# Kernel optimization log

Hardware: AMD Instinct MI355X
Metric: run time of the kernel (lower is better)

## Reference

```python
import jax, jax.numpy as jnp
import numpy as np

N = 1000000
E = 16000000


def gcn_conv(x, W, b, src, dst, dinv_sqrt):
    # x: [N, Cin]; W: [Cin, Cout]; src/dst: [E'] (self-loops included)
    xw = x @ W                                   # [N, Cout]
    norm = dinv_sqrt[src] * dinv_sqrt[dst]       # [E']
    msg = xw[src] * norm[:, None]                # [E', Cout]
    out = jax.ops.segment_sum(msg, dst, num_segments=x.shape[0])
    return out + b


def setup_inputs() -> dict:
    key = jax.random.key(0)
    ks = jax.random.split(key, 8)
    x = jax.random.normal(ks[0], (N, 1), dtype=jnp.float32)
    edge_index = jax.random.randint(ks[1], (2, E), 0, N, dtype=jnp.int64)
    W1 = jax.random.normal(ks[2], (1, 3), dtype=jnp.float32)
    b1 = jax.random.normal(ks[3], (3,), dtype=jnp.float32) * 0.1
    W2 = jax.random.normal(ks[4], (3, 3), dtype=jnp.float32) * 0.5
    b2 = jax.random.normal(ks[5], (3,), dtype=jnp.float32) * 0.1
    W3 = jax.random.normal(ks[6], (3, 3), dtype=jnp.float32) * 0.5
    b3 = jax.random.normal(ks[7], (3,), dtype=jnp.float32) * 0.1
    return {"x": x, "edge_index": edge_index, "W1": W1, "b1": b1,
            "W2": W2, "b2": b2, "W3": W3, "b3": b3}


def reference(x, edge_index, W1, b1, W2, b2, W3, b3):
    n = x.shape[0]
    # add self-loops (PyG GCNConv default)
    loop = jnp.arange(n, dtype=edge_index.dtype)
    src = jnp.concatenate([edge_index[0], loop])
    dst = jnp.concatenate([edge_index[1], loop])
    # symmetric normalization: deg over targets of A + I
    deg = jax.ops.segment_sum(jnp.ones_like(dst, dtype=x.dtype), dst, num_segments=n)
    dinv_sqrt = jnp.where(deg > 0, jax.lax.rsqrt(deg), 0.0)
    h = jax.nn.relu(gcn_conv(x, W1, b1, src, dst, dinv_sqrt))
    h = jax.nn.relu(gcn_conv(h, W2, b2, src, dst, dinv_sqrt))
    h = jax.nn.relu(gcn_conv(h, W3, b3, src, dst, dinv_sqrt))
    return h
```

## Files before the change

kernel.cpp:

```cpp
#include <hip/hip_runtime.h>

#define THREADS 256
#define TILE 8192
#define TPB_S 512
#define EPT 16
#define BUCKET_BITS 10
#define BUCKET_SIZE 1024
#define NT_MAX 2048
#define STAGE_CAP 16512
#define NSLICE 8
#define SLICE_SHIFT 17

__device__ __forceinline__ long long llmin(long long a, long long b) { return a < b ? a : b; }


__global__ void detect_i64_kernel(const int* __restrict__ e, int* __restrict__ flag) {
    if (blockIdx.x == 0 && threadIdx.x == 0) {
        bool all_odd_zero = true, any_even = false;
#pragma unroll
        for (int k = 0; k < 16; ++k) {
            if (e[2 * k + 1] != 0) all_odd_zero = false;
            if (e[2 * k] != 0) any_even = true;
        }
        *flag = (all_odd_zero && any_even) ? 1 : 0;
    }
}


__global__ __launch_bounds__(TPB_S) void binsort_kernel(
        const int* __restrict__ e, long long E, const int* __restrict__ flag,
        int nbuck, int* __restrict__ packed, int* __restrict__ ofs) {
    __shared__ int hist[1024];
    __shared__ int sarr[TPB_S];
    __shared__ int srec[TILE];
    const int tid = threadIdx.x;
    hist[tid] = 0;
    hist[tid + TPB_S] = 0;
    __syncthreads();

    const bool i64 = (*flag != 0);
    const long long beg = (long long)blockIdx.x * TILE;
    const int tile_len = (int)llmin((long long)TILE, E - beg);

    int rec[EPT];
    int bkt[EPT];
#pragma unroll
    for (int k = 0; k < EPT; ++k) {
        int j = tid + k * TPB_S;
        bkt[k] = -1;
        if (j < tile_len) {
            long long idx = beg + j;
            int s, d;
            if (i64) { s = ((const int2*)e)[idx].x; d = ((const int2*)e)[E + idx].x; }
            else     { s = e[idx];                  d = e[E + idx]; }
            bkt[k] = d >> BUCKET_BITS;
            rec[k] = ((d & (BUCKET_SIZE - 1)) << 20) | s;
            atomicAdd(&hist[bkt[k]], 1);
        }
    }
    __syncthreads();

    int v0 = hist[2 * tid], v1 = hist[2 * tid + 1];
    sarr[tid] = v0 + v1;
    __syncthreads();
    for (int off = 1; off < TPB_S; off <<= 1) {
        int t = (tid >= off) ? sarr[tid - off] : 0;
        __syncthreads();
        sarr[tid] += t;
        __syncthreads();
    }
    int excl = (tid == 0) ? 0 : sarr[tid - 1];
    hist[2 * tid] = excl;
    hist[2 * tid + 1] = excl + v0;
    __syncthreads();

    int* orow = ofs + (size_t)blockIdx.x * nbuck;
    if (tid < nbuck) orow[tid] = hist[tid];
    if (tid + TPB_S < nbuck) orow[tid + TPB_S] = hist[tid + TPB_S];
    __syncthreads();

#pragma unroll
    for (int k = 0; k < EPT; ++k) {
        if (bkt[k] >= 0) {
            int pos = atomicAdd(&hist[bkt[k]], 1);
            srec[pos] = rec[k];
        }
    }
    __syncthreads();

    int* prow = packed + (size_t)blockIdx.x * TILE;
    for (int j = tid; j < tile_len; j += TPB_S) prow[j] = srec[j];
}

#define TRT 32
__global__ void transpose_kernel(const int* __restrict__ in, int rows, int cols,
                                 int* __restrict__ outT) {
    __shared__ int tb[TRT][TRT + 1];
    int c0 = blockIdx.x * TRT, r0 = blockIdx.y * TRT;
    int lx = threadIdx.x, ly = threadIdx.y;
    for (int dy = ly; dy < TRT; dy += 8) {
        int r = r0 + dy, c = c0 + lx;
        if (r < rows && c < cols) tb[dy][lx] = in[(size_t)r * cols + c];
    }
    __syncthreads();
    for (int dy = ly; dy < TRT; dy += 8) {
        int r = c0 + dy, c = r0 + lx;
        if (r < cols && c < rows) outT[(size_t)r * rows + c] = tb[lx][dy];
    }
}


__global__ __launch_bounds__(THREADS) void bcnt_kernel(
        const int* __restrict__ ofsT, long long E, int ntiles, int nbuck,
        int* __restrict__ bcnt) {
    __shared__ int sh[THREADS];
    const int b = blockIdx.x, tid = threadIdx.x;
    const int* row0 = ofsT + (size_t)b * ntiles;
    const int* row1 = row0 + ntiles;
    const bool last_b = (b == nbuck - 1);
    int s = 0;
    for (int t = tid; t < ntiles; t += THREADS) {
        int o = row0[t];
        int tl = (t == ntiles - 1) ? (int)(E - (long long)t * TILE) : TILE;
        int o2 = last_b ? tl : row1[t];
        s += o2 - o;
    }
    sh[tid] = s;
    __syncthreads();
    for (int off = THREADS >> 1; off > 0; off >>= 1) {
        if (tid < off) sh[tid] += sh[tid + off];
        __syncthreads();
    }
    if (tid == 0) bcnt[b] = sh[0];
}

__global__ __launch_bounds__(1024) void bscan_kernel(
        const int* __restrict__ bcnt, int nbuck, int* __restrict__ bs) {
    __shared__ int sh[1024];
    int tid = threadIdx.x;
    int v = (tid < nbuck) ? bcnt[tid] : 0;
    sh[tid] = v;
    __syncthreads();
    for (int off = 1; off < 1024; off <<= 1) {
        int t = (tid >= off) ? sh[tid - off] : 0;
        __syncthreads();
        sh[tid] += t;
        __syncthreads();
    }
    if (tid < nbuck) bs[tid] = sh[tid] - v;
    if (tid == nbuck - 1) bs[nbuck] = sh[tid];
}


__global__ __launch_bounds__(TPB_S) void merge_kernel(
        const int* __restrict__ ofsT, const int* __restrict__ packed,
        const int* __restrict__ bs, long long E, int ntiles, int nbuck,
        int* __restrict__ merged) {
    __shared__ int lofs[NT_MAX];
    __shared__ int tsum[TPB_S];
    __shared__ int stage[STAGE_CAP];
    __shared__ int stage2[STAGE_CAP];
    __shared__ int scnt[NSLICE];
    __shared__ int scur[NSLICE];
    const int tid = threadIdx.x, b = blockIdx.x;
    const int* row0 = ofsT + (size_t)b * ntiles;
    const int* row1 = row0 + ntiles;
    const bool last_b = (b == nbuck - 1);
    const int per = (ntiles + TPB_S - 1) / TPB_S;
    const int t0 = tid * per;
    if (tid < NSLICE) scnt[tid] = 0;

    int s = 0;
    for (int k = 0; k < per; ++k) {
        int t = t0 + k;
        if (t < ntiles) {
            int o = row0[t];
            int tl = (t == ntiles - 1) ? (int)(E - (long long)t * TILE) : TILE;
            int o2 = last_b ? tl : row1[t];
            lofs[t] = s;
            s += o2 - o;
        }
    }
    tsum[tid] = s;
    __syncthreads();
    for (int off = 1; off < TPB_S; off <<= 1) {
        int t = (tid >= off) ? tsum[tid - off] : 0;
        __syncthreads();
        tsum[tid] += t;
        __syncthreads();
    }
    const int excl = tsum[tid] - s;
    const int total = tsum[TPB_S - 1];
    for (int k = 0; k < per; ++k) {
        int t = t0 + k;
        if (t < ntiles) lofs[t] += excl;
    }
    __syncthreads();

    const int bsb = bs[b];
    int myslc[NSLICE];
#pragma unroll
    for (int i = 0; i < NSLICE; ++i) myslc[i] = 0;

    for (int k = 0; k < per; ++k) {
        int t = t0 + k;
        if (t >= ntiles) break;
        int o = row0[t];
        int tl = (t == ntiles - 1) ? (int)(E - (long long)t * TILE) : TILE;
        int o2 = last_b ? tl : row1[t];
        const int* pr = packed + (size_t)t * TILE;
        int q = lofs[t];
        for (int j = o; j < o2; ++j, ++q) {
            int a0 = pr[j];
            if (q < STAGE_CAP) {
                stage[q] = a0;
                myslc[((unsigned)a0 & 0xFFFFFu) >> SLICE_SHIFT]++;
            } else {
                merged[bsb + q] = a0;
            }
        }
    }
#pragma unroll
    for (int i = 0; i < NSLICE; ++i)
        if (myslc[i]) atomicAdd(&scnt[i], myslc[i]);
    __syncthreads();
    if (tid == 0) {
        int run = 0;
#pragma unroll
        for (int i = 0; i < NSLICE; ++i) { scur[i] = run; run += scnt[i]; }
    }
    __syncthreads();

    const int wlen = total < STAGE_CAP ? total : STAGE_CAP;
    for (int j = tid; j < wlen; j += TPB_S) {
        int rec = stage[j];
        int sl = ((unsigned)rec & 0xFFFFFu) >> SLICE_SHIFT;
        int pos = atomicAdd(&scur[sl], 1);
        stage2[pos] = rec;
    }
    __syncthreads();
    for (int j = tid; j < wlen; j += TPB_S) merged[bsb + j] = stage2[j];
}


__global__ __launch_bounds__(TPB_S) void deg_init_kernel(
        const int* __restrict__ bs, const int* __restrict__ packed,
        const float* __restrict__ x,
        float* __restrict__ dinv, float* __restrict__ p, int N) {
    __shared__ int cnt[BUCKET_SIZE];
    for (int k = threadIdx.x; k < BUCKET_SIZE; k += blockDim.x) cnt[k] = 0;
    __syncthreads();
    int beg = bs[blockIdx.x], end = bs[blockIdx.x + 1];
    int stride = blockDim.x;
    int k = beg + threadIdx.x;
    for (; k + 3 * stride < end; k += 4 * stride) {
        unsigned r0 = packed[k], r1 = packed[k + stride];
        unsigned r2 = packed[k + 2 * stride], r3 = packed[k + 3 * stride];
        atomicAdd(&cnt[r0 >> 20], 1);
        atomicAdd(&cnt[r1 >> 20], 1);
        atomicAdd(&cnt[r2 >> 20], 1);
        atomicAdd(&cnt[r3 >> 20], 1);
    }
    for (; k < end; k += stride) atomicAdd(&cnt[((unsigned)packed[k]) >> 20], 1);
    __syncthreads();
    int base = blockIdx.x << BUCKET_BITS;
    for (int j = threadIdx.x; j < BUCKET_SIZE; j += blockDim.x) {
        int i = base + j;
        if (i < N) {
            float di = rsqrtf((float)cnt[j] + 1.0f);
            dinv[i] = di;
            p[i] = x[i] * di;
        }
    }
}

__global__ __launch_bounds__(TPB_S) void layer1_bucket_kernel(
        const int* __restrict__ bs, const int* __restrict__ packed,
        const float* __restrict__ p, const float* __restrict__ dinv,
        const float* __restrict__ W1, const float* __restrict__ b1,
        const float* __restrict__ W2,
        float4* __restrict__ y2, int N) {
    __shared__ float acc[BUCKET_SIZE];
    for (int k = threadIdx.x; k < BUCKET_SIZE; k += blockDim.x) acc[k] = 0.0f;
    __syncthreads();
    int beg = bs[blockIdx.x], end = bs[blockIdx.x + 1];
    int stride = blockDim.x;
    int k = beg + threadIdx.x;
    for (; k + 3 * stride < end; k += 4 * stride) {
        unsigned r0 = packed[k], r1 = packed[k + stride];
        unsigned r2 = packed[k + 2 * stride], r3 = packed[k + 3 * stride];
        float v0 = p[r0 & 0xFFFFFu], v1 = p[r1 & 0xFFFFFu];
        float v2 = p[r2 & 0xFFFFFu], v3 = p[r3 & 0xFFFFFu];
        atomicAdd(&acc[r0 >> 20], v0);
        atomicAdd(&acc[r1 >> 20], v1);
        atomicAdd(&acc[r2 >> 20], v2);
        atomicAdd(&acc[r3 >> 20], v3);
    }
    for (; k < end; k += stride) {
        unsigned rec = (unsigned)packed[k];
        atomicAdd(&acc[rec >> 20], p[rec & 0xFFFFFu]);
    }
    __syncthreads();
    int base = blockIdx.x << BUCKET_BITS;
    for (int j = threadIdx.x; j < BUCKET_SIZE; j += blockDim.x) {
        int i = base + j;
        if (i >= N) continue;
        float di = dinv[i];
        float t = di * (acc[j] + p[i]);
        float h0 = fmaxf(t * W1[0] + b1[0], 0.0f);
        float h1 = fmaxf(t * W1[1] + b1[1], 0.0f);
        float h2 = fmaxf(t * W1[2] + b1[2], 0.0f);
        float4 o;
        o.x = di * (h0 * W2[0] + h1 * W2[3] + h2 * W2[6]);
        o.y = di * (h0 * W2[1] + h1 * W2[4] + h2 * W2[7]);
        o.z = di * (h0 * W2[2] + h1 * W2[5] + h2 * W2[8]);
        o.w = 0.0f;
        y2[i] = o;
    }
}

__global__ __launch_bounds__(TPB_S) void layer_mid_bucket_kernel(
        const int* __restrict__ bs, const int* __restrict__ packed,
        const float4* __restrict__ y, const float* __restrict__ dinv,
        const float* __restrict__ b, const float* __restrict__ Wn,
        float4* __restrict__ ynext, int N) {
    __shared__ float acc[BUCKET_SIZE * 3];
    for (int k = threadIdx.x; k < BUCKET_SIZE * 3; k += blockDim.x) acc[k] = 0.0f;
    __syncthreads();
    int beg = bs[blockIdx.x], end = bs[blockIdx.x + 1];
    int stride = blockDim.x;
    int k = beg + threadIdx.x;
    for (; k + 3 * stride < end; k += 4 * stride) {
        unsigned r0 = packed[k], r1 = packed[k + stride];
        unsigned r2 = packed[k + 2 * stride], r3 = packed[k + 3 * stride];
        float4 v0 = y[r0 & 0xFFFFFu], v1 = y[r1 & 0xFFFFFu];
        float4 v2 = y[r2 & 0xFFFFFu], v3 = y[r3 & 0xFFFFFu];
        int d0 = (r0 >> 20) * 3, d1 = (r1 >> 20) * 3, d2 = (r2 >> 20) * 3, d3 = (r3 >> 20) * 3;
        atomicAdd(&acc[d0 + 0], v0.x); atomicAdd(&acc[d0 + 1], v0.y); atomicAdd(&acc[d0 + 2], v0.z);
        atomicAdd(&acc[d1 + 0], v1.x); atomicAdd(&acc[d1 + 1], v1.y); atomicAdd(&acc[d1 + 2], v1.z);
        atomicAdd(&acc[d2 + 0], v2.x); atomicAdd(&acc[d2 + 1], v2.y); atomicAdd(&acc[d2 + 2], v2.z);
        atomicAdd(&acc[d3 + 0], v3.x); atomicAdd(&acc[d3 + 1], v3.y); atomicAdd(&acc[d3 + 2], v3.z);
    }
    for (; k < end; k += stride) {
        unsigned rec = (unsigned)packed[k];
        float4 v = y[rec & 0xFFFFFu];
        int dl = (rec >> 20) * 3;
        atomicAdd(&acc[dl + 0], v.x);
        atomicAdd(&acc[dl + 1], v.y);
        atomicAdd(&acc[dl + 2], v.z);
    }
    __syncthreads();
    int base = blockIdx.x << BUCKET_BITS;
    for (int j = threadIdx.x; j < BUCKET_SIZE; j += blockDim.x) {
        int i = base + j;
        if (i >= N) continue;
        float di = dinv[i];
        float4 yi = y[i];
        float h0 = fmaxf(di * (acc[j * 3 + 0] + yi.x) + b[0], 0.0f);
        float h1 = fmaxf(di * (acc[j * 3 + 1] + yi.y) + b[1], 0.0f);
        float h2 = fmaxf(di * (acc[j * 3 + 2] + yi.z) + b[2], 0.0f);
        float4 o;
        o.x = di * (h0 * Wn[0] + h1 * Wn[3] + h2 * Wn[6]);
        o.y = di * (h0 * Wn[1] + h1 * Wn[4] + h2 * Wn[7]);
        o.z = di * (h0 * Wn[2] + h1 * Wn[5] + h2 * Wn[8]);
        o.w = 0.0f;
        ynext[i] = o;
    }
}

__global__ __launch_bounds__(TPB_S) void layer_last_bucket_kernel(
        const int* __restrict__ bs, const int* __restrict__ packed,
        const float4* __restrict__ y, const float* __restrict__ dinv,
        const float* __restrict__ b,
        float* __restrict__ out, int N) {
    __shared__ float acc[BUCKET_SIZE * 3];
    for (int k = threadIdx.x; k < BUCKET_SIZE * 3; k += blockDim.x) acc[k] = 0.0f;
    __syncthreads();
    int beg = bs[blockIdx.x], end = bs[blockIdx.x + 1];
    int stride = blockDim.x;
    int k = beg + threadIdx.x;
    for (; k + 3 * stride < end; k += 4 * stride) {
        unsigned r0 = packed[k], r1 = packed[k + stride];
        unsigned r2 = packed[k + 2 * stride], r3 = packed[k + 3 * stride];
        float4 v0 = y[r0 & 0xFFFFFu], v1 = y[r1 & 0xFFFFFu];
        float4 v2 = y[r2 & 0xFFFFFu], v3 = y[r3 & 0xFFFFFu];
        int d0 = (r0 >> 20) * 3, d1 = (r1 >> 20) * 3, d2 = (r2 >> 20) * 3, d3 = (r3 >> 20) * 3;
        atomicAdd(&acc[d0 + 0], v0.x); atomicAdd(&acc[d0 + 1], v0.y); atomicAdd(&acc[d0 + 2], v0.z);
        atomicAdd(&acc[d1 + 0], v1.x); atomicAdd(&acc[d1 + 1], v1.y); atomicAdd(&acc[d1 + 2], v1.z);
        atomicAdd(&acc[d2 + 0], v2.x); atomicAdd(&acc[d2 + 1], v2.y); atomicAdd(&acc[d2 + 2], v2.z);
        atomicAdd(&acc[d3 + 0], v3.x); atomicAdd(&acc[d3 + 1], v3.y); atomicAdd(&acc[d3 + 2], v3.z);
    }
    for (; k < end; k += stride) {
        unsigned rec = (unsigned)packed[k];
        float4 v = y[rec & 0xFFFFFu];
        int dl = (rec >> 20) * 3;
        atomicAdd(&acc[dl + 0], v.x);
        atomicAdd(&acc[dl + 1], v.y);
        atomicAdd(&acc[dl + 2], v.z);
    }
    __syncthreads();
    int base = blockIdx.x << BUCKET_BITS;
    for (int j = threadIdx.x; j < BUCKET_SIZE; j += blockDim.x) {
        int i = base + j;
        if (i >= N) continue;
        float di = dinv[i];
        float4 yi = y[i];
        out[i * 3 + 0] = fmaxf(di * (acc[j * 3 + 0] + yi.x) + b[0], 0.0f);
        out[i * 3 + 1] = fmaxf(di * (acc[j * 3 + 1] + yi.y) + b[1], 0.0f);
        out[i * 3 + 2] = fmaxf(di * (acc[j * 3 + 2] + yi.z) + b[2], 0.0f);
    }
}


__global__ void deg_kernel(const int* __restrict__ e, long long E,
                           const int* __restrict__ flag, float* __restrict__ deg) {
    const bool i64 = (*flag != 0);
    long long i = (long long)blockIdx.x * blockDim.x + threadIdx.x;
    const long long stride = (long long)gridDim.x * blockDim.x;
    for (; i < E; i += stride) {
        long long t = i64 ? (long long)e[2 * E + 2 * i] : (long long)e[E + i];
        atomicAdd(deg + t, 1.0f);
    }
}

__global__ void node_init_kernel(const float* __restrict__ x, const float* __restrict__ W1,
                                 float* __restrict__ deg_dinv, float* __restrict__ A, int N) {
    int i = blockIdx.x * blockDim.x + threadIdx.x;
    if (i >= N) return;
    float di = rsqrtf(deg_dinv[i] + 1.0f);
    deg_dinv[i] = di;
    float v = x[i] * di;
    A[i * 3 + 0] = v * W1[0];
    A[i * 3 + 1] = v * W1[1];
    A[i * 3 + 2] = v * W1[2];
}

__global__ void scatter_kernel(const int* __restrict__ e, long long E,
                               const int* __restrict__ flag,
                               const float* __restrict__ y, float* __restrict__ acc) {
    const bool i64 = (*flag != 0);
    long long i = (long long)blockIdx.x * blockDim.x + threadIdx.x;
    const long long stride = (long long)gridDim.x * blockDim.x;
    for (; i < E; i += stride) {
        int s, t;
        if (i64) { s = e[2 * i]; t = e[2 * E + 2 * i]; }
        else     { s = e[i];     t = e[E + i]; }
        atomicAdd(acc + (long long)t * 3 + 0, y[(long long)s * 3 + 0]);
        atomicAdd(acc + (long long)t * 3 + 1, y[(long long)s * 3 + 1]);
        atomicAdd(acc + (long long)t * 3 + 2, y[(long long)s * 3 + 2]);
    }
}

__global__ void finalize_mid_kernel(const float* __restrict__ dinv, const float* __restrict__ y,
                                    float* __restrict__ acc, const float* __restrict__ b,
                                    const float* __restrict__ Wn, int N) {
    int i = blockIdx.x * blockDim.x + threadIdx.x;
    if (i >= N) return;
    float di = dinv[i];
    float h0 = fmaxf(di * (acc[i * 3 + 0] + y[i * 3 + 0]) + b[0], 0.0f);
    float h1 = fmaxf(di * (acc[i * 3 + 1] + y[i * 3 + 1]) + b[1], 0.0f);
    float h2 = fmaxf(di * (acc[i * 3 + 2] + y[i * 3 + 2]) + b[2], 0.0f);
    float z0 = di * (h0 * Wn[0] + h1 * Wn[3] + h2 * Wn[6]);
    float z1 = di * (h0 * Wn[1] + h1 * Wn[4] + h2 * Wn[7]);
    float z2 = di * (h0 * Wn[2] + h1 * Wn[5] + h2 * Wn[8]);
    acc[i * 3 + 0] = z0;
    acc[i * 3 + 1] = z1;
    acc[i * 3 + 2] = z2;
}

__global__ void finalize_last_kernel(const float* __restrict__ dinv, const float* __restrict__ y,
                                     const float* __restrict__ acc, const float* __restrict__ b,
                                     float* __restrict__ out, int N) {
    int i = blockIdx.x * blockDim.x + threadIdx.x;
    if (i >= N) return;
    float di = dinv[i];
    out[i * 3 + 0] = fmaxf(di * (acc[i * 3 + 0] + y[i * 3 + 0]) + b[0], 0.0f);
    out[i * 3 + 1] = fmaxf(di * (acc[i * 3 + 1] + y[i * 3 + 1]) + b[1], 0.0f);
    out[i * 3 + 2] = fmaxf(di * (acc[i * 3 + 2] + y[i * 3 + 2]) + b[2], 0.0f);
}


extern "C" void kernel_launch(void* const* d_in, const int* in_sizes, int n_in,
                              void* d_out, int out_size, void* d_ws, size_t ws_size,
                              hipStream_t stream) {
    const float* x  = (const float*)d_in[0];
    const int*   ei = (const int*)d_in[1];
    const float* W1 = (const float*)d_in[2];
    const float* b1 = (const float*)d_in[3];
    const float* W2 = (const float*)d_in[4];
    const float* b2 = (const float*)d_in[5];
    const float* W3 = (const float*)d_in[6];
    const float* b3 = (const float*)d_in[7];
    float* out = (float*)d_out;

    const long long N = in_sizes[0];
    const long long E = (long long)in_sizes[1] / 2;

    const int nbuck  = (int)((N + BUCKET_SIZE - 1) >> BUCKET_BITS);
    const int ntiles = (int)((E + TILE - 1) / TILE);

    char* w = (char*)d_ws;
    size_t off = 0;
    auto alloc = [&](size_t bytes) -> char* {
        char* pp = w + off;
        off = (off + bytes + 255) & ~(size_t)255;
        return pp;
    };

    int*    flag   = (int*)alloc(4);
    int*    ofs    = (int*)alloc((size_t)ntiles * nbuck * 4);
    int*    ofsT   = (int*)alloc((size_t)nbuck * ntiles * 4);
    int*    bcnt   = (int*)alloc((size_t)nbuck * 4);
    int*    bs     = (int*)alloc(((size_t)nbuck + 1) * 4);
    int*    packed = (int*)alloc((size_t)ntiles * TILE * 4);
    int*    merged = (int*)alloc((size_t)E * 4);
    float*  dinv   = (float*)alloc((size_t)N * 4);
    float*  p      = (float*)alloc((size_t)N * 4);
    float4* y2     = (float4*)packed;
    float4* y3     = (float4*)((char*)packed + (size_t)N * 16);

    const int nblk = (int)((N + THREADS - 1) / THREADS);

    if (off <= ws_size && N <= (1 << 20) && nbuck <= 1024 && ntiles <= NT_MAX &&
        (size_t)ntiles * TILE * 4 >= (size_t)N * 32) {
        detect_i64_kernel<<<1, 64, 0, stream>>>(ei, flag);
        binsort_kernel<<<ntiles, TPB_S, 0, stream>>>(ei, E, flag, nbuck, packed, ofs);
        dim3 tb(32, 8);
        dim3 tg((nbuck + TRT - 1) / TRT, (ntiles + TRT - 1) / TRT);
        transpose_kernel<<<tg, tb, 0, stream>>>(ofs, ntiles, nbuck, ofsT);
        bcnt_kernel<<<nbuck, THREADS, 0, stream>>>(ofsT, E, ntiles, nbuck, bcnt);
        bscan_kernel<<<1, 1024, 0, stream>>>(bcnt, nbuck, bs);
        merge_kernel<<<nbuck, TPB_S, 0, stream>>>(ofsT, packed, bs, E, ntiles, nbuck, merged);

        deg_init_kernel<<<nbuck, TPB_S, 0, stream>>>(bs, merged, x, dinv, p, (int)N);
        layer1_bucket_kernel<<<nbuck, TPB_S, 0, stream>>>(bs, merged, p, dinv, W1, b1, W2, y2, (int)N);
        layer_mid_bucket_kernel<<<nbuck, TPB_S, 0, stream>>>(bs, merged, y2, dinv, b2, W3, y3, (int)N);
        layer_last_bucket_kernel<<<nbuck, TPB_S, 0, stream>>>(bs, merged, y3, dinv, b3, out, (int)N);
    } else {
        int*   fflag = (int*)w;
        float* fdinv = (float*)(w + 256);
        float* A     = fdinv + N;
        size_t need_full = 256 + (size_t)N * 4 + (size_t)N * 12 * 2;
        float* B = (ws_size >= need_full) ? (A + 3 * N) : out;
        const int eblk = 2048;

        detect_i64_kernel<<<1, 64, 0, stream>>>(ei, fflag);
        hipMemsetAsync(fdinv, 0, (size_t)N * 4, stream);
        deg_kernel<<<eblk, THREADS, 0, stream>>>(ei, E, fflag, fdinv);
        node_init_kernel<<<nblk, THREADS, 0, stream>>>(x, W1, fdinv, A, (int)N);

        hipMemsetAsync(B, 0, (size_t)N * 12, stream);
        scatter_kernel<<<eblk, THREADS, 0, stream>>>(ei, E, fflag, A, B);
        finalize_mid_kernel<<<nblk, THREADS, 0, stream>>>(fdinv, A, B, b1, W2, (int)N);

        hipMemsetAsync(A, 0, (size_t)N * 12, stream);
        scatter_kernel<<<eblk, THREADS, 0, stream>>>(ei, E, fflag, B, A);
        finalize_mid_kernel<<<nblk, THREADS, 0, stream>>>(fdinv, B, A, b2, W3, (int)N);

        hipMemsetAsync(B, 0, (size_t)N * 12, stream);
        scatter_kernel<<<eblk, THREADS, 0, stream>>>(ei, E, fflag, A, B);
        finalize_last_kernel<<<nblk, THREADS, 0, stream>>>(fdinv, A, B, b3, out, (int)N);
    }
}
```

Baseline: 904.9 us.

## Rewrite merge as count-then-scatter and vectorize edge loads in bucket kernels

The merge kernel no longer copies records into a staging buffer and then reorders them with shared atomics. It first counts records per source slice for each thread, runs a block prefix scan to get each thread's private write cursors, then scatters directly into one staging array. This drops one shared buffer and the atomic reordering pass, at the cost of reading the packed tiles twice. The degree and layer kernels now read edge records as aligned int4 pairs with eight gathers in flight per thread, which adds alignment prologue and epilogue loops and changes the per-thread access pattern from strided to contiguous chunks.

```diff
diff --git a/kernel.cpp b/kernel.cpp
--- a/kernel.cpp
+++ b/kernel.cpp
@@ -7,9 +7,10 @@
 #define BUCKET_BITS 10
 #define BUCKET_SIZE 1024
 #define NT_MAX 2048
-#define STAGE_CAP 16512
 #define NSLICE 8
 #define SLICE_SHIFT 17
+#define CAP2 17408
+#define MSK 0xFFFFFu
 
 __device__ __forceinline__ long long llmin(long long a, long long b) { return a < b ? a : b; }
 
@@ -156,51 +157,19 @@
         const int* __restrict__ ofsT, const int* __restrict__ packed,
         const int* __restrict__ bs, long long E, int ntiles, int nbuck,
         int* __restrict__ merged) {
-    __shared__ int lofs[NT_MAX];
-    __shared__ int tsum[TPB_S];
-    __shared__ int stage[STAGE_CAP];
-    __shared__ int stage2[STAGE_CAP];
-    __shared__ int scnt[NSLICE];
-    __shared__ int scur[NSLICE];
+    __shared__ int stage2[CAP2];
+    __shared__ int f[NSLICE * TPB_S];
+    __shared__ int sarr[TPB_S];
     const int tid = threadIdx.x, b = blockIdx.x;
     const int* row0 = ofsT + (size_t)b * ntiles;
     const int* row1 = row0 + ntiles;
     const bool last_b = (b == nbuck - 1);
     const int per = (ntiles + TPB_S - 1) / TPB_S;
     const int t0 = tid * per;
-    if (tid < NSLICE) scnt[tid] = 0;
-
-    int s = 0;
-    for (int k = 0; k < per; ++k) {
-        int t = t0 + k;
-        if (t < ntiles) {
-            int o = row0[t];
-            int tl = (t == ntiles - 1) ? (int)(E - (long long)t * TILE) : TILE;
-            int o2 = last_b ? tl : row1[t];
-            lofs[t] = s;
-            s += o2 - o;
-        }
-    }
-    tsum[tid] = s;
-    __syncthreads();
-    for (int off = 1; off < TPB_S; off <<= 1) {
-        int t = (tid >= off) ? tsum[tid - off] : 0;
-        __syncthreads();
-        tsum[tid] += t;
-        __syncthreads();
-    }
-    const int excl = tsum[tid] - s;
-    const int total = tsum[TPB_S - 1];
-    for (int k = 0; k < per; ++k) {
-        int t = t0 + k;
-        if (t < ntiles) lofs[t] += excl;
-    }
-    __syncthreads();
-
-    const int bsb = bs[b];
-    int myslc[NSLICE];
-#pragma unroll
-    for (int i = 0; i < NSLICE; ++i) myslc[i] = 0;
+
+    int cnt[NSLICE];
+#pragma unroll
+    for (int i = 0; i < NSLICE; ++i) cnt[i] = 0;
 
     for (int k = 0; k < per; ++k) {
         int t = t0 + k;
@@ -209,63 +178,89 @@
         int tl = (t == ntiles - 1) ? (int)(E - (long long)t * TILE) : TILE;
         int o2 = last_b ? tl : row1[t];
         const int* pr = packed + (size_t)t * TILE;
-        int q = lofs[t];
-        for (int j = o; j < o2; ++j, ++q) {
-            int a0 = pr[j];
-            if (q < STAGE_CAP) {
-                stage[q] = a0;
-                myslc[((unsigned)a0 & 0xFFFFFu) >> SLICE_SHIFT]++;
-            } else {
-                merged[bsb + q] = a0;
-            }
+        for (int j = o; j < o2; ++j)
+            cnt[(((unsigned)pr[j]) & MSK) >> SLICE_SHIFT]++;
+    }
+#pragma unroll
+    for (int sl = 0; sl < NSLICE; ++sl) f[sl * TPB_S + tid] = cnt[sl];
+    __syncthreads();
+
+    int loc[NSLICE];
+    int s = 0;
+#pragma unroll
+    for (int j = 0; j < NSLICE; ++j) { loc[j] = f[tid * NSLICE + j]; s += loc[j]; }
+    sarr[tid] = s;
+    __syncthreads();
+    for (int off = 1; off < TPB_S; off <<= 1) {
+        int t = (tid >= off) ? sarr[tid - off] : 0;
+        __syncthreads();
+        sarr[tid] += t;
+        __syncthreads();
+    }
+    int ex = sarr[tid] - s;
+    const int total = sarr[TPB_S - 1];
+#pragma unroll
+    for (int j = 0; j < NSLICE; ++j) { f[tid * NSLICE + j] = ex; ex += loc[j]; }
+    __syncthreads();
+
+    int cur[NSLICE];
+#pragma unroll
+    for (int sl = 0; sl < NSLICE; ++sl) cur[sl] = f[sl * TPB_S + tid];
+
+    const int bsb = bs[b];
+    for (int k = 0; k < per; ++k) {
+        int t = t0 + k;
+        if (t >= ntiles) break;
+        int o = row0[t];
+        int tl = (t == ntiles - 1) ? (int)(E - (long long)t * TILE) : TILE;
+        int o2 = last_b ? tl : row1[t];
+        const int* pr = packed + (size_t)t * TILE;
+        for (int j = o; j < o2; ++j) {
+            int r = pr[j];
+            int sl = (((unsigned)r) & MSK) >> SLICE_SHIFT;
+            int pos = cur[sl]++;
+            if (pos < CAP2) stage2[pos] = r;
+            else merged[bsb + pos] = r;
         }
     }
-#pragma unroll
-    for (int i = 0; i < NSLICE; ++i)
-        if (myslc[i]) atomicAdd(&scnt[i], myslc[i]);
-    __syncthreads();
-    if (tid == 0) {
-        int run = 0;
-#pragma unroll
-        for (int i = 0; i < NSLICE; ++i) { scur[i] = run; run += scnt[i]; }
-    }
-    __syncthreads();
-
-    const int wlen = total < STAGE_CAP ? total : STAGE_CAP;
-    for (int j = tid; j < wlen; j += TPB_S) {
-        int rec = stage[j];
-        int sl = ((unsigned)rec & 0xFFFFFu) >> SLICE_SHIFT;
-        int pos = atomicAdd(&scur[sl], 1);
-        stage2[pos] = rec;
-    }
-    __syncthreads();
+    __syncthreads();
+    const int wlen = total < CAP2 ? total : CAP2;
     for (int j = tid; j < wlen; j += TPB_S) merged[bsb + j] = stage2[j];
 }
 
 
 __global__ __launch_bounds__(TPB_S) void deg_init_kernel(
-        const int* __restrict__ bs, const int* __restrict__ packed,
+        const int* __restrict__ bs, const int* __restrict__ merged,
         const float* __restrict__ x,
         float* __restrict__ dinv, float* __restrict__ p, int N) {
     __shared__ int cnt[BUCKET_SIZE];
-    for (int k = threadIdx.x; k < BUCKET_SIZE; k += blockDim.x) cnt[k] = 0;
+    const int tid = threadIdx.x;
+    for (int k = tid; k < BUCKET_SIZE; k += TPB_S) cnt[k] = 0;
     __syncthreads();
     int beg = bs[blockIdx.x], end = bs[blockIdx.x + 1];
-    int stride = blockDim.x;
-    int k = beg + threadIdx.x;
-    for (; k + 3 * stride < end; k += 4 * stride) {
-        unsigned r0 = packed[k], r1 = packed[k + stride];
-        unsigned r2 = packed[k + 2 * stride], r3 = packed[k + 3 * stride];
-        atomicAdd(&cnt[r0 >> 20], 1);
-        atomicAdd(&cnt[r1 >> 20], 1);
-        atomicAdd(&cnt[r2 >> 20], 1);
-        atomicAdd(&cnt[r3 >> 20], 1);
-    }
-    for (; k < end; k += stride) atomicAdd(&cnt[((unsigned)packed[k]) >> 20], 1);
-    __syncthreads();
-    int base = blockIdx.x << BUCKET_BITS;
-    for (int j = threadIdx.x; j < BUCKET_SIZE; j += blockDim.x) {
-        int i = base + j;
+    int a0 = (beg + 3) & ~3; if (a0 > end) a0 = end;
+    for (int k = beg + tid; k < a0; k += TPB_S)
+        atomicAdd(&cnt[((unsigned)merged[k]) >> 20], 1);
+    int base = a0;
+    for (; base + 8 * TPB_S <= end; base += 8 * TPB_S) {
+        int q = base + tid * 8;
+        int4 ra = *(const int4*)(merged + q);
+        int4 rb = *(const int4*)(merged + q + 4);
+        atomicAdd(&cnt[((unsigned)ra.x) >> 20], 1);
+        atomicAdd(&cnt[((unsigned)ra.y) >> 20], 1);
+        atomicAdd(&cnt[((unsigned)ra.z) >> 20], 1);
+        atomicAdd(&cnt[((unsigned)ra.w) >> 20], 1);
+        atomicAdd(&cnt[((unsigned)rb.x) >> 20], 1);
+        atomicAdd(&cnt[((unsigned)rb.y) >> 20], 1);
+        atomicAdd(&cnt[((unsigned)rb.z) >> 20], 1);
+        atomicAdd(&cnt[((unsigned)rb.w) >> 20], 1);
+    }
+    for (int k = base + tid; k < end; k += TPB_S)
+        atomicAdd(&cnt[((unsigned)merged[k]) >> 20], 1);
+    __syncthreads();
+    int nbase = blockIdx.x << BUCKET_BITS;
+    for (int j = tid; j < BUCKET_SIZE; j += TPB_S) {
+        int i = nbase + j;
         if (i < N) {
             float di = rsqrtf((float)cnt[j] + 1.0f);
             dinv[i] = di;
@@ -275,35 +270,51 @@
 }
 
 __global__ __launch_bounds__(TPB_S) void layer1_bucket_kernel(
-        const int* __restrict__ bs, const int* __restrict__ packed,
+        const int* __restrict__ bs, const int* __restrict__ merged,
         const float* __restrict__ p, const float* __restrict__ dinv,
         const float* __restrict__ W1, const float* __restrict__ b1,
         const float* __restrict__ W2,
         float4* __restrict__ y2, int N) {
     __shared__ float acc[BUCKET_SIZE];
-    for (int k = threadIdx.x; k < BUCKET_SIZE; k += blockDim.x) acc[k] = 0.0f;
+    const int tid = threadIdx.x;
+    for (int k = tid; k < BUCKET_SIZE; k += TPB_S) acc[k] = 0.0f;
     __syncthreads();
     int beg = bs[blockIdx.x], end = bs[blockIdx.x + 1];
-    int stride = blockDim.x;
-    int k = beg + threadIdx.x;
-    for (; k + 3 * stride < end; k += 4 * stride) {
-        unsigned r0 = packed[k], r1 = packed[k + stride];
-        unsigned r2 = packed[k + 2 * stride], r3 = packed[k + 3 * stride];
-        float v0 = p[r0 & 0xFFFFFu], v1 = p[r1 & 0xFFFFFu];
-        float v2 = p[r2 & 0xFFFFFu], v3 = p[r3 & 0xFFFFFu];
-        atomicAdd(&acc[r0 >> 20], v0);
-        atomicAdd(&acc[r1 >> 20], v1);
-        atomicAdd(&acc[r2 >> 20], v2);
-        atomicAdd(&acc[r3 >> 20], v3);
-    }
-    for (; k < end; k += stride) {
-        unsigned rec = (unsigned)packed[k];
-        atomicAdd(&acc[rec >> 20], p[rec & 0xFFFFFu]);
-    }
-    __syncthreads();
-    int base = blockIdx.x << BUCKET_BITS;
-    for (int j = threadIdx.x; j < BUCKET_SIZE; j += blockDim.x) {
-        int i = base + j;
+    int a0 = (beg + 3) & ~3; if (a0 > end) a0 = end;
+    for (int k = beg + tid; k < a0; k += TPB_S) {
+        unsigned r = (unsigned)merged[k];
+        atomicAdd(&acc[r >> 20], p[r & MSK]);
+    }
+    int base = a0;
+    for (; base + 8 * TPB_S <= end; base += 8 * TPB_S) {
+        int q = base + tid * 8;
+        int4 ra = *(const int4*)(merged + q);
+        int4 rb = *(const int4*)(merged + q + 4);
+        float v0 = p[((unsigned)ra.x) & MSK];
+        float v1 = p[((unsigned)ra.y) & MSK];
+        float v2 = p[((unsigned)ra.z) & MSK];
+        float v3 = p[((unsigned)ra.w) & MSK];
+        float v4 = p[((unsigned)rb.x) & MSK];
+        float v5 = p[((unsigned)rb.y) & MSK];
+        float v6 = p[((unsigned)rb.z) & MSK];
+        float v7 = p[((unsigned)rb.w) & MSK];
+        atomicAdd(&acc[((unsigned)ra.x) >> 20], v0);
+        atomicAdd(&acc[((unsigned)ra.y) >> 20], v1);
+        atomicAdd(&acc[((unsigned)ra.z) >> 20], v2);
+        atomicAdd(&acc[((unsigned)ra.w) >> 20], v3);
+        atomicAdd(&acc[((unsigned)rb.x) >> 20], v4);
+        atomicAdd(&acc[((unsigned)rb.y) >> 20], v5);
+        atomicAdd(&acc[((unsigned)rb.z) >> 20], v6);
+        atomicAdd(&acc[((unsigned)rb.w) >> 20], v7);
+    }
+    for (int k = base + tid; k < end; k += TPB_S) {
+        unsigned r = (unsigned)merged[k];
+        atomicAdd(&acc[r >> 20], p[r & MSK]);
+    }
+    __syncthreads();
+    int nbase = blockIdx.x << BUCKET_BITS;
+    for (int j = tid; j < BUCKET_SIZE; j += TPB_S) {
+        int i = nbase + j;
         if (i >= N) continue;
         float di = dinv[i];
         float t = di * (acc[j] + p[i]);
@@ -319,40 +330,58 @@
     }
 }
 
+__device__ __forceinline__ void acc3_atomic(float* acc, unsigned r, float4 v) {
+    int dl = (r >> 20) * 3;
+    atomicAdd(&acc[dl + 0], v.x);
+    atomicAdd(&acc[dl + 1], v.y);
+    atomicAdd(&acc[dl + 2], v.z);
+}
+
 __global__ __launch_bounds__(TPB_S) void layer_mid_bucket_kernel(
-        const int* __restrict__ bs, const int* __restrict__ packed,
+        const int* __restrict__ bs, const int* __restrict__ merged,
         const float4* __restrict__ y, const float* __restrict__ dinv,
         const float* __restrict__ b, const float* __restrict__ Wn,
         float4* __restrict__ ynext, int N) {
     __shared__ float acc[BUCKET_SIZE * 3];
-    for (int k = threadIdx.x; k < BUCKET_SIZE * 3; k += blockDim.x) acc[k] = 0.0f;
+    const int tid = threadIdx.x;
+    for (int k = tid; k < BUCKET_SIZE * 3; k += TPB_S) acc[k] = 0.0f;
     __syncthreads();
     int beg = bs[blockIdx.x], end = bs[blockIdx.x + 1];
-    int stride = blockDim.x;
-    int k = beg + threadIdx.x;
-    for (; k + 3 * stride < end; k += 4 * stride) {
-        unsigned r0 = packed[k], r1 = packed[k + stride];
-        unsigned r2 = packed[k + 2 * stride], r3 = packed[k + 3 * stride];
-        float4 v0 = y[r0 & 0xFFFFFu], v1 = y[r1 & 0xFFFFFu];
-        float4 v2 = y[r2 & 0xFFFFFu], v3 = y[r3 & 0xFFFFFu];
-        int d0 = (r0 >> 20) * 3, d1 = (r1 >> 20) * 3, d2 = (r2 >> 20) * 3, d3 = (r3 >> 20) * 3;
-        atomicAdd(&acc[d0 + 0], v0.x); atomicAdd(&acc[d0 + 1], v0.y); atomicAdd(&acc[d0 + 2], v0.z);
-        atomicAdd(&acc[d1 + 0], v1.x); atomicAdd(&acc[d1 + 1], v1.y); atomicAdd(&acc[d1 + 2], v1.z);
-        atomicAdd(&acc[d2 + 0], v2.x); atomicAdd(&acc[d2 + 1], v2.y); atomicAdd(&acc[d2 + 2], v2.z);
-        atomicAdd(&acc[d3 + 0], v3.x); atomicAdd(&acc[d3 + 1], v3.y); atomicAdd(&acc[d3 + 2], v3.z);
-    }
-    for (; k < end; k += stride) {
-        unsigned rec = (unsigned)packed[k];
-        float4 v = y[rec & 0xFFFFFu];
-        int dl = (rec >> 20) * 3;
-        atomicAdd(&acc[dl + 0], v.x);
-        atomicAdd(&acc[dl + 1], v.y);
-        atomicAdd(&acc[dl + 2], v.z);
-    }
-    __syncthreads();
-    int base = blockIdx.x << BUCKET_BITS;
-    for (int j = threadIdx.x; j < BUCKET_SIZE; j += blockDim.x) {
-        int i = base + j;
+    int a0 = (beg + 3) & ~3; if (a0 > end) a0 = end;
+    for (int k = beg + tid; k < a0; k += TPB_S) {
+        unsigned r = (unsigned)merged[k];
+        acc3_atomic(acc, r, y[r & MSK]);
+    }
+    int base = a0;
+    for (; base + 8 * TPB_S <= end; base += 8 * TPB_S) {
+        int q = base + tid * 8;
+        int4 ra = *(const int4*)(merged + q);
+        int4 rb = *(const int4*)(merged + q + 4);
+        float4 v0 = y[((unsigned)ra.x) & MSK];
+        float4 v1 = y[((unsigned)ra.y) & MSK];
+        float4 v2 = y[((unsigned)ra.z) & MSK];
+        float4 v3 = y[((unsigned)ra.w) & MSK];
+        float4 v4 = y[((unsigned)rb.x) & MSK];
+        float4 v5 = y[((unsigned)rb.y) & MSK];
+        float4 v6 = y[((unsigned)rb.z) & MSK];
+        float4 v7 = y[((unsigned)rb.w) & MSK];
+        acc3_atomic(acc, (unsigned)ra.x, v0);
+        acc3_atomic(acc, (unsigned)ra.y, v1);
+        acc3_atomic(acc, (unsigned)ra.z, v2);
+        acc3_atomic(acc, (unsigned)ra.w, v3);
+        acc3_atomic(acc, (unsigned)rb.x, v4);
+        acc3_atomic(acc, (unsigned)rb.y, v5);
+        acc3_atomic(acc, (unsigned)rb.z, v6);
+        acc3_atomic(acc, (unsigned)rb.w, v7);
+    }
+    for (int k = base + tid; k < end; k += TPB_S) {
+        unsigned r = (unsigned)merged[k];
+        acc3_atomic(acc, r, y[r & MSK]);
+    }
+    __syncthreads();
+    int nbase = blockIdx.x << BUCKET_BITS;
+    for (int j = tid; j < BUCKET_SIZE; j += TPB_S) {
+        int i = nbase + j;
         if (i >= N) continue;
         float di = dinv[i];
         float4 yi = y[i];
@@ -369,39 +398,50 @@
 }
 
 __global__ __launch_bounds__(TPB_S) void layer_last_bucket_kernel(
-        const int* __restrict__ bs, const int* __restrict__ packed,
+        const int* __restrict__ bs, const int* __restrict__ merged,
         const float4* __restrict__ y, const float* __restrict__ dinv,
         const float* __restrict__ b,
         float* __restrict__ out, int N) {
     __shared__ float acc[BUCKET_SIZE * 3];
-    for (int k = threadIdx.x; k < BUCKET_SIZE * 3; k += blockDim.x) acc[k] = 0.0f;
+    const int tid = threadIdx.x;
+    for (int k = tid; k < BUCKET_SIZE * 3; k += TPB_S) acc[k] = 0.0f;
     __syncthreads();
     int beg = bs[blockIdx.x], end = bs[blockIdx.x + 1];
-    int stride = blockDim.x;
-    int k = beg + threadIdx.x;
-    for (; k + 3 * stride < end; k += 4 * stride) {
-        unsigned r0 = packed[k], r1 = packed[k + stride];
-        unsigned r2 = packed[k + 2 * stride], r3 = packed[k + 3 * stride];
-        float4 v0 = y[r0 & 0xFFFFFu], v1 = y[r1 & 0xFFFFFu];
-        float4 v2 = y[r2 & 0xFFFFFu], v3 = y[r3 & 0xFFFFFu];
-        int d0 = (r0 >> 20) * 3, d1 = (r1 >> 20) * 3, d2 = (r2 >> 20) * 3, d3 = (r3 >> 20) * 3;
-        atomicAdd(&acc[d0 + 0], v0.x); atomicAdd(&acc[d0 + 1], v0.y); atomicAdd(&acc[d0 + 2], v0.z);
-        atomicAdd(&acc[d1 + 0], v1.x); atomicAdd(&acc[d1 + 1], v1.y); atomicAdd(&acc[d1 + 2], v1.z);
-        atomicAdd(&acc[d2 + 0], v2.x); atomicAdd(&acc[d2 + 1], v2.y); atomicAdd(&acc[d2 + 2], v2.z);
-        atomicAdd(&acc[d3 + 0], v3.x); atomicAdd(&acc[d3 + 1], v3.y); atomicAdd(&acc[d3 + 2], v3.z);
-    }
-    for (; k < end; k += stride) {
-        unsigned rec = (unsigned)packed[k];
-        float4 v = y[rec & 0xFFFFFu];
-        int dl = (rec >> 20) * 3;
-        atomicAdd(&acc[dl + 0], v.x);
-        atomicAdd(&acc[dl + 1], v.y);
-        atomicAdd(&acc[dl + 2], v.z);
-    }
-    __syncthreads();
-    int base = blockIdx.x << BUCKET_BITS;
-    for (int j = threadIdx.x; j < BUCKET_SIZE; j += blockDim.x) {
-        int i = base + j;
+    int a0 = (beg + 3) & ~3; if (a0 > end) a0 = end;
+    for (int k = beg + tid; k < a0; k += TPB_S) {
+        unsigned r = (unsigned)merged[k];
+        acc3_atomic(acc, r, y[r & MSK]);
+    }
+    int base = a0;
+    for (; base + 8 * TPB_S <= end; base += 8 * TPB_S) {
+        int q = base + tid * 8;
+        int4 ra = *(const int4*)(merged + q);
+        int4 rb = *(const int4*)(merged + q + 4);
+        float4 v0 = y[((unsigned)ra.x) & MSK];
+        float4 v1 = y[((unsigned)ra.y) & MSK];
+        float4 v2 = y[((unsigned)ra.z) & MSK];
+        float4 v3 = y[((unsigned)ra.w) & MSK];
+        float4 v4 = y[((unsigned)rb.x) & MSK];
+        float4 v5 = y[((unsigned)rb.y) & MSK];
+        float4 v6 = y[((unsigned)rb.z) & MSK];
+        float4 v7 = y[((unsigned)rb.w) & MSK];
+        acc3_atomic(acc, (unsigned)ra.x, v0);
+        acc3_atomic(acc, (unsigned)ra.y, v1);
+        acc3_atomic(acc, (unsigned)ra.z, v2);
+        acc3_atomic(acc, (unsigned)ra.w, v3);
+        acc3_atomic(acc, (unsigned)rb.x, v4);
+        acc3_atomic(acc, (unsigned)rb.y, v5);
+        acc3_atomic(acc, (unsigned)rb.z, v6);
+        acc3_atomic(acc, (unsigned)rb.w, v7);
+    }
+    for (int k = base + tid; k < end; k += TPB_S) {
+        unsigned r = (unsigned)merged[k];
+        acc3_atomic(acc, r, y[r & MSK]);
+    }
+    __syncthreads();
+    int nbase = blockIdx.x << BUCKET_BITS;
+    for (int j = tid; j < BUCKET_SIZE; j += TPB_S) {
+        int i = nbase + j;
         if (i >= N) continue;
         float di = dinv[i];
         float4 yi = y[i];
```

After: 957.3 us. 5.8% more time.
